# Kernel optimization log

Measured on AMD Instinct MI355X. Metric: run time of the kernel, lower is better.

The kernel has to match this reference:

```python
import jax, jax.numpy as jnp
import numpy as np

F = 26          # field_size
D = 16          # embed_dim
B = 16384       # batch
VOCABS = [1000] * F
OFFSETS = np.concatenate([[0], np.cumsum(VOCABS)[:-1]]).astype(np.int32)
IU, JU = np.triu_indices(F, k=1)   # 325 pairs (i<j)
P = IU.shape[0]
BN_EPS = 1e-3   # Keras BatchNormalization default epsilon


def setup_inputs() -> dict:
    key = jax.random.key(0)
    ks = jax.random.split(key, 8)
    s = 0.05  # keras 'random_normal' initializer stddev
    return {
        "x": jax.random.randint(ks[0], (B, F), 0, 1000, dtype=jnp.int32),
        "emb_table": jax.random.normal(ks[1], (sum(VOCABS) + 1, D), jnp.float32) * s,
        "se_w1": jax.random.normal(ks[2], (F, F // 2), jnp.float32) * s,
        "se_w2": jax.random.normal(ks[3], (F // 2, F), jnp.float32) * s,
        "bl_w": jax.random.normal(ks[4], (P, D, D), jnp.float32) * s,
        "w1": jax.random.normal(ks[5], (F * (F - 1) * D, 64), jnp.float32) * s,
        "b1": jnp.zeros((64,), jnp.float32),
        "g1": jnp.ones((64,), jnp.float32),
        "be1": jnp.zeros((64,), jnp.float32),
        "m1": jnp.zeros((64,), jnp.float32),
        "v1": jnp.ones((64,), jnp.float32),
        "w2": jax.random.normal(ks[6], (64, 32), jnp.float32) * s,
        "b2": jnp.zeros((32,), jnp.float32),
        "g2": jnp.ones((32,), jnp.float32),
        "be2": jnp.zeros((32,), jnp.float32),
        "m2": jnp.zeros((32,), jnp.float32),
        "v2": jnp.ones((32,), jnp.float32),
        "w3": jax.random.normal(ks[7], (32, 1), jnp.float32) * s,
        "b3": jnp.zeros((1,), jnp.float32),
    }


def _bilinear(v, bl_w):
    # v: [B, F, D]; shared W stack over the 325 ordered pairs (i<j)
    # tmp[p] = (v_i @ W_p) * v_j  -> [B, P, D]
    return jnp.einsum('bpd,pde->bpe', v[:, IU], bl_w) * v[:, JU]


def _bn(h, g, b, m, v):
    return g * (h - m) * jax.lax.rsqrt(v + BN_EPS) + b


def reference(x, emb_table, se_w1, se_w2, bl_w,
              w1, b1, g1, be1, m1, v1,
              w2, b2, g2, be2, m2, v2,
              w3, b3):
    ids = x + jnp.asarray(OFFSETS)
    e = emb_table[ids]                         # [B, F, D]
    # SE layer: mean-pool over embed dim, two ReLU dense layers, rescale
    z = e.mean(axis=-1)                        # [B, F]
    A = jax.nn.relu(jax.nn.relu(z @ se_w1) @ se_w2)
    se = e * A[..., None]                      # [B, F, D]
    # Bilinear interaction (same weights for both calls)
    p = _bilinear(e, bl_w).reshape(e.shape[0], -1)     # [B, P*D]
    se_p = _bilinear(se, bl_w).reshape(e.shape[0], -1)
    h = jnp.concatenate([p, se_p], axis=-1)    # [B, F*(F-1)*D]
    # MLP with inference-mode BatchNorm; dropout=0 is a no-op
    h = jax.nn.relu(_bn(h @ w1 + b1, g1, be1, m1, v1))
    h = jax.nn.relu(_bn(h @ w2 + b2, g2, be2, m2, v2))
    return jax.nn.sigmoid(h @ w3 + b3)         # [B, 1]
```

## Files before the change

kernel.cpp:

```cpp
#include <hip/hip_runtime.h>
#include <cstdint>
#include <cstddef>


#define F_FIELDS 26
#define P_PAIRS 325
#define PAD_PAIRS 336
#define BATCH 16384
#define BN_EPS 1e-3f
#define ROWS 64

typedef short bf16x8 __attribute__((ext_vector_type(8)));
typedef float f32x4 __attribute__((ext_vector_type(4)));
typedef int   i32x4 __attribute__((ext_vector_type(4)));

struct PairTab { unsigned char iu[PAD_PAIRS]; unsigned char ju[PAD_PAIRS]; };
static constexpr PairTab make_pairs() {
    PairTab t{};
    int p = 0;
    for (int a = 0; a < F_FIELDS; ++a)
        for (int b = a + 1; b < F_FIELDS; ++b) { t.iu[p] = (unsigned char)a; t.ju[p] = (unsigned char)b; ++p; }
    for (; p < PAD_PAIRS; ++p) { t.iu[p] = 0; t.ju[p] = 0; }
    return t;
}
__constant__ PairTab PT = make_pairs();

__device__ __forceinline__ unsigned short bf16u(float v) {
    unsigned u = __float_as_uint(v);
    unsigned r = (u + 0x7fffu + ((u >> 16) & 1u)) >> 16;
    return (unsigned short)r;
}
__device__ __forceinline__ unsigned pk_bf16(float lo, float hi) {
    return (unsigned)bf16u(lo) | ((unsigned)bf16u(hi) << 16);
}
__device__ __forceinline__ float bflo(unsigned d) { return __uint_as_float(d << 16); }
__device__ __forceinline__ float bfhi(unsigned d) { return __uint_as_float(d & 0xffff0000u); }
__device__ __forceinline__ unsigned pk_trunc(float u, float cu) {
    return __builtin_amdgcn_perm(__float_as_uint(cu), __float_as_uint(u), 0x07060302u);
}

__global__ __launch_bounds__(256) void k_wprep(const float* __restrict__ w1,
        const float* __restrict__ blw, unsigned short* __restrict__ w1catL,
        unsigned short* __restrict__ wcatL) {
    const int p = blockIdx.x;
    const int tid = threadIdx.x;
    if (p >= P_PAIRS) {
        int4 z = make_int4(0, 0, 0, 0);
        *(int4*)(w1catL + (size_t)p * 2048 + tid * 8) = z;
        if (tid < 64) *(int4*)(wcatL + (size_t)p * 512 + tid * 8) = z;
        return;
    }
    __shared__ float wu[1024], wv[1024], wb[256];
    ((float4*)wu)[tid] = ((const float4*)(w1 + (size_t)p * 1024))[tid];
    ((float4*)wv)[tid] = ((const float4*)(w1 + 332800 + (size_t)p * 1024))[tid];
    if (tid < 64) ((float4*)wb)[tid] = ((const float4*)(blw + (size_t)p * 256))[tid];
    __syncthreads();
    {
        int nt = tid >> 6, lane = tid & 63, ln = lane & 15, q = lane >> 4;
        int o = nt * 16 + ln;
        unsigned short outv[8];
        #pragma unroll
        for (int j = 0; j < 8; ++j) {
            int k = q * 8 + j, d = k >> 1, su = k & 1;
            outv[j] = bf16u(su ? wv[d * 64 + o] : wu[d * 64 + o]);
        }
        *(int4*)(w1catL + (size_t)p * 2048 + tid * 8) = *(const int4*)outv;
    }
    if (tid < 64) {
        int ln = tid & 15, q = tid >> 4;
        unsigned short outv[8];
        #pragma unroll
        for (int j = 0; j < 8; ++j) {
            int din = q * 8 + j;
            outv[j] = (din < 16) ? bf16u(wb[din * 16 + ln]) : (unsigned short)0;
        }
        *(int4*)(wcatL + (size_t)p * 512 + tid * 8) = *(const int4*)outv;
    }
}

union __align__(16) SMem {
    struct {
        unsigned short eS[ROWS * 424];
        float aS[F_FIELDS * ROWS];
    } a;
    struct {
        unsigned ysh[8 * 8 * 64 * 4];
        float h1s[ROWS * 65];
        float h2s[ROWS * 36];
    } b;
};

#define ISSUE_W(pp, waS, wbS0, wbS1, wbS2, wbS3) do {                                   \
    const unsigned short* ba_ = wcatL + (size_t)(pp) * 512 + lane * 8;                  \
    const unsigned short* bb_ = w1catL + (size_t)(pp) * 2048 + lane * 8;                \
    asm volatile("global_load_dwordx4 %0, %1, off"             : "=v"(waS)  : "v"(ba_)); \
    asm volatile("global_load_dwordx4 %0, %1, off"             : "=v"(wbS0) : "v"(bb_)); \
    asm volatile("global_load_dwordx4 %0, %1, off offset:1024" : "=v"(wbS1) : "v"(bb_)); \
    asm volatile("global_load_dwordx4 %0, %1, off offset:2048" : "=v"(wbS2) : "v"(bb_)); \
    asm volatile("global_load_dwordx4 %0, %1, off offset:3072" : "=v"(wbS3) : "v"(bb_)); \
} while (0)

#define PAIR_BODY(p_, waS, wbS0, wbS1, wbS2, wbS3, waT, wbT0, wbT1, wbT2, wbT3) do {    \
    const int pn_ = ((p_) + 1 < p1) ? (p_) + 1 : (p1 - 1);                              \
    const int pf_ = ((p_) + 2 < p1) ? (p_) + 2 : (p1 - 1);                              \
    const int ju_ = PT.ju[p_];                                                          \
    uint2 ejv_[4]; float cv_[4];                                                        \
    _Pragma("unroll") for (int mt = 0; mt < 4; ++mt) {                                  \
        ejv_[mt] = *(const uint2*)(eS + (mt * 16 + ln) * 424 + ju_ * 16 + q * 4);       \
        cv_[mt]  = ai[mt] * aS[ju_ * ROWS + mt * 16 + ln];                              \
    }                                                                                   \
    const int iun_ = PT.iu[pn_];                                                        \
    if (iun_ != iu_c) {                                                                 \
        iu_c = iun_;                                                                    \
        _Pragma("unroll") for (int mt = 0; mt < 4; ++mt) {                              \
            eiB[mt] = __builtin_bit_cast(bf16x8,                                        \
                *(const int4*)(eS + (mt * 16 + ln) * 424 + iu_c * 16 + (q & 1) * 8));   \
            ai[mt] = aS[iu_c * ROWS + mt * 16 + ln];                                    \
        }                                                                               \
    }                                                                                   \
    bf16x8 wbv_[4] = { __builtin_bit_cast(bf16x8, wbS0), __builtin_bit_cast(bf16x8, wbS1), \
                       __builtin_bit_cast(bf16x8, wbS2), __builtin_bit_cast(bf16x8, wbS3) }; \
    _Pragma("unroll") for (int mt = 0; mt < 4; ++mt) {                                  \
        f32x4 t = tc[mt];                                                               \
        float e0 = bflo(ejv_[mt].x), e1 = bfhi(ejv_[mt].x);                             \
        float e2 = bflo(ejv_[mt].y), e3 = bfhi(ejv_[mt].y);                             \
        float c  = cv_[mt];                                                             \
        float u0 = t[0] * e0, u1 = t[1] * e1, u2 = t[2] * e2, u3 = t[3] * e3;           \
        int4 af;                                                                        \
        af.x = (int)pk_trunc(u0, c * u0);                                               \
        af.y = (int)pk_trunc(u1, c * u1);                                               \
        af.z = (int)pk_trunc(u2, c * u2);                                               \
        af.w = (int)pk_trunc(u3, c * u3);                                               \
        bf16x8 A_ = __builtin_bit_cast(bf16x8, af);                                     \
        _Pragma("unroll") for (int nt = 0; nt < 4; ++nt)                                \
            acc[mt][nt] = __builtin_amdgcn_mfma_f32_16x16x32_bf16(A_, wbv_[nt], acc[mt][nt], 0, 0, 0); \
    }                                                                                   \
    ISSUE_W(pf_, waS, wbS0, wbS1, wbS2, wbS3);                                          \
    asm volatile("s_waitcnt vmcnt(5)" ::: "memory");                                    \
    __builtin_amdgcn_sched_barrier(0);                                                  \
    {                                                                                   \
        bf16x8 waT_ = __builtin_bit_cast(bf16x8, waT);                                  \
        _Pragma("unroll") for (int mt = 0; mt < 4; ++mt)                                \
            tc[mt] = __builtin_amdgcn_mfma_f32_16x16x32_bf16(waT_, eiB[mt], zero4, 0, 0, 0); \
    }                                                                                   \
} while (0)

__global__ __launch_bounds__(512, 2) void k_main(const int* __restrict__ x,
        const float* __restrict__ emb, const float* __restrict__ sw1,
        const float* __restrict__ sw2, const unsigned short* __restrict__ w1catL,
        const unsigned short* __restrict__ wcatL,
        const float* __restrict__ b1, const float* __restrict__ g1,
        const float* __restrict__ be1, const float* __restrict__ m1,
        const float* __restrict__ v1,
        const float* __restrict__ w2, const float* __restrict__ b2,
        const float* __restrict__ g2, const float* __restrict__ be2,
        const float* __restrict__ m2, const float* __restrict__ v2,
        const float* __restrict__ w3, const float* __restrict__ b3,
        float* __restrict__ out) {
    __shared__ SMem sm;
    __shared__ float z_s[ROWS][F_FIELDS];
    __shared__ float sw1_s[F_FIELDS * 13];
    __shared__ float sw2_s[13 * F_FIELDS];
    const int tid = threadIdx.x;
    const int b0 = blockIdx.x * ROWS;
    unsigned short* eS = sm.a.eS;
    float* aS = sm.a.aS;

    for (int i = tid; i < F_FIELDS * 13; i += 512) { sw1_s[i] = sw1[i]; sw2_s[i] = sw2[i]; }
    for (int idx = tid; idx < ROWS * F_FIELDS; idx += 512) {
        int r = idx / F_FIELDS, f = idx - r * F_FIELDS;
        int id = x[(b0 + r) * F_FIELDS + f] + f * 1000;
        const float4* src = (const float4*)(emb + (size_t)id * 16);
        float4 v0 = src[0], v1l = src[1], v2l = src[2], v3l = src[3];
        int4 o0, o1;
        o0.x = (int)pk_bf16(v0.x, v0.y);  o0.y = (int)pk_bf16(v0.z, v0.w);
        o0.z = (int)pk_bf16(v1l.x, v1l.y); o0.w = (int)pk_bf16(v1l.z, v1l.w);
        o1.x = (int)pk_bf16(v2l.x, v2l.y); o1.y = (int)pk_bf16(v2l.z, v2l.w);
        o1.z = (int)pk_bf16(v3l.x, v3l.y); o1.w = (int)pk_bf16(v3l.z, v3l.w);
        *(int4*)(eS + r * 424 + f * 16) = o0;
        *(int4*)(eS + r * 424 + f * 16 + 8) = o1;
        float s = v0.x + v0.y + v0.z + v0.w + v1l.x + v1l.y + v1l.z + v1l.w
                + v2l.x + v2l.y + v2l.z + v2l.w + v3l.x + v3l.y + v3l.z + v3l.w;
        z_s[r][f] = s * (1.0f / 16.0f);
    }
    __syncthreads();
    if (tid < ROWS) {
        float s1[13];
        #pragma unroll
        for (int o = 0; o < 13; ++o) {
            float acc0 = 0.f;
            #pragma unroll
            for (int f = 0; f < F_FIELDS; ++f) acc0 = fmaf(z_s[tid][f], sw1_s[f * 13 + o], acc0);
            s1[o] = fmaxf(acc0, 0.0f);
        }
        #pragma unroll
        for (int f = 0; f < F_FIELDS; ++f) {
            float acc0 = 0.f;
            #pragma unroll
            for (int o = 0; o < 13; ++o) acc0 = fmaf(s1[o], sw2_s[o * F_FIELDS + f], acc0);
            aS[f * ROWS + tid] = fmaxf(acc0, 0.0f);
        }
    }
    __syncthreads();

    const int w    = tid >> 6;
    const int lane = tid & 63;
    const int ln   = lane & 15;
    const int q    = lane >> 4;
    const int p0 = w * 42, p1 = p0 + 42;

    f32x4 acc[4][4];
    #pragma unroll
    for (int a = 0; a < 4; ++a)
        #pragma unroll
        for (int b = 0; b < 4; ++b) acc[a][b] = (f32x4){0.f, 0.f, 0.f, 0.f};
    const f32x4 zero4 = {0.f, 0.f, 0.f, 0.f};

    int iu_c = PT.iu[p0];
    bf16x8 eiB[4];
    float ai[4];
    #pragma unroll
    for (int mt = 0; mt < 4; ++mt) {
        eiB[mt] = __builtin_bit_cast(bf16x8,
            *(const int4*)(eS + (mt * 16 + ln) * 424 + iu_c * 16 + (q & 1) * 8));
        ai[mt] = aS[iu_c * ROWS + mt * 16 + ln];
    }

    i32x4 waA, wbA0, wbA1, wbA2, wbA3;
    i32x4 waB, wbB0, wbB1, wbB2, wbB3;
    ISSUE_W(p0,     waA, wbA0, wbA1, wbA2, wbA3);
    ISSUE_W(p0 + 1, waB, wbB0, wbB1, wbB2, wbB3);
    asm volatile("s_waitcnt vmcnt(5)" ::: "memory");
    __builtin_amdgcn_sched_barrier(0);

    f32x4 tc[4];
    {
        bf16x8 waA_ = __builtin_bit_cast(bf16x8, waA);
        #pragma unroll
        for (int mt = 0; mt < 4; ++mt)
            tc[mt] = __builtin_amdgcn_mfma_f32_16x16x32_bf16(waA_, eiB[mt], zero4, 0, 0, 0);
    }

    for (int p = p0; p < p1; p += 2) {
        PAIR_BODY(p,     waA, wbA0, wbA1, wbA2, wbA3, waB, wbB0, wbB1, wbB2, wbB3);
        PAIR_BODY(p + 1, waB, wbB0, wbB1, wbB2, wbB3, waA, wbA0, wbA1, wbA2, wbA3);
    }
    asm volatile("s_waitcnt vmcnt(0)" ::: "memory");
    __builtin_amdgcn_sched_barrier(0);

    __syncthreads();
    unsigned* ysh = sm.b.ysh;
    float* h1s = sm.b.h1s;
    float* h2s = sm.b.h2s;
    #pragma unroll
    for (int mt = 0; mt < 4; ++mt)
        #pragma unroll
        for (int nh = 0; nh < 2; ++nh) {
            int nt0 = nh * 2, nt1 = nh * 2 + 1;
            int4 v;
            v.x = (int)pk_bf16(acc[mt][nt0][0], acc[mt][nt0][1]);
            v.y = (int)pk_bf16(acc[mt][nt0][2], acc[mt][nt0][3]);
            v.z = (int)pk_bf16(acc[mt][nt1][0], acc[mt][nt1][1]);
            v.w = (int)pk_bf16(acc[mt][nt1][2], acc[mt][nt1][3]);
            *(int4*)(ysh + ((w * 8 + mt * 2 + nh) * 64 + lane) * 4) = v;
        }
    __syncthreads();

    {
        const int s = tid >> 6, lane2 = tid & 63, ln2 = lane2 & 15, q2 = lane2 >> 4;
        const int mt = s >> 1, nh = s & 1;
        const int c0 = nh * 32 + ln2, c1 = c0 + 16;
        const float sc0 = g1[c0] * rsqrtf(v1[c0] + BN_EPS);
        const float of0 = be1[c0] + sc0 * (b1[c0] - m1[c0]);
        const float sc1 = g1[c1] * rsqrtf(v1[c1] + BN_EPS);
        const float of1 = be1[c1] + sc1 * (b1[c1] - m1[c1]);
        float s8[8];
        #pragma unroll
        for (int i = 0; i < 8; ++i) s8[i] = 0.f;
        #pragma unroll
        for (int wv = 0; wv < 8; ++wv) {
            int4 v = *(const int4*)(ysh + ((wv * 8 + s) * 64 + lane2) * 4);
            s8[0] += bflo((unsigned)v.x); s8[1] += bfhi((unsigned)v.x);
            s8[2] += bflo((unsigned)v.y); s8[3] += bfhi((unsigned)v.y);
            s8[4] += bflo((unsigned)v.z); s8[5] += bfhi((unsigned)v.z);
            s8[6] += bflo((unsigned)v.w); s8[7] += bfhi((unsigned)v.w);
        }
        const int row0 = mt * 16 + q2 * 4;
        #pragma unroll
        for (int r = 0; r < 4; ++r) {
            h1s[(row0 + r) * 65 + c0] = fmaxf(s8[r] * sc0 + of0, 0.f);
            h1s[(row0 + r) * 65 + c1] = fmaxf(s8[4 + r] * sc1 + of1, 0.f);
        }
    }
    __syncthreads();

    {
        const int row = tid >> 3, gg = tid & 7;
        const int o0 = gg * 4;
        float a0 = 0.f, a1 = 0.f, a2 = 0.f, a3 = 0.f;
        #pragma unroll 8
        for (int k = 0; k < 64; ++k) {
            float hk = h1s[row * 65 + k];
            float4 wv = *(const float4*)(w2 + k * 32 + o0);
            a0 = fmaf(hk, wv.x, a0);
            a1 = fmaf(hk, wv.y, a1);
            a2 = fmaf(hk, wv.z, a2);
            a3 = fmaf(hk, wv.w, a3);
        }
        const float4 g2v  = *(const float4*)(g2 + o0);
        const float4 b2v  = *(const float4*)(b2 + o0);
        const float4 m2v  = *(const float4*)(m2 + o0);
        const float4 v2v  = *(const float4*)(v2 + o0);
        const float4 be2v = *(const float4*)(be2 + o0);
        float4 hv;
        hv.x = fmaxf(g2v.x * (a0 + b2v.x - m2v.x) * rsqrtf(v2v.x + BN_EPS) + be2v.x, 0.f);
        hv.y = fmaxf(g2v.y * (a1 + b2v.y - m2v.y) * rsqrtf(v2v.y + BN_EPS) + be2v.y, 0.f);
        hv.z = fmaxf(g2v.z * (a2 + b2v.z - m2v.z) * rsqrtf(v2v.z + BN_EPS) + be2v.z, 0.f);
        hv.w = fmaxf(g2v.w * (a3 + b2v.w - m2v.w) * rsqrtf(v2v.w + BN_EPS) + be2v.w, 0.f);
        *(float4*)(h2s + row * 36 + o0) = hv;
    }
    __syncthreads();
    if (tid < ROWS) {
        float sacc = b3[0];
        #pragma unroll
        for (int k = 0; k < 32; ++k) sacc = fmaf(h2s[tid * 36 + k], w3[k], sacc);
        out[b0 + tid] = 1.0f / (1.0f + expf(-sacc));
    }
}

extern "C" void kernel_launch(void* const* d_in, const int* in_sizes, int n_in,
                              void* d_out, int out_size, void* d_ws, size_t ws_size,
                              hipStream_t stream) {
    const int*   x   = (const int*)d_in[0];
    const float* emb = (const float*)d_in[1];
    const float* sw1 = (const float*)d_in[2];
    const float* sw2 = (const float*)d_in[3];
    const float* blw = (const float*)d_in[4];
    const float* w1  = (const float*)d_in[5];
    const float* b1  = (const float*)d_in[6];
    const float* g1  = (const float*)d_in[7];
    const float* be1 = (const float*)d_in[8];
    const float* m1  = (const float*)d_in[9];
    const float* v1  = (const float*)d_in[10];
    const float* w2  = (const float*)d_in[11];
    const float* b2  = (const float*)d_in[12];
    const float* g2  = (const float*)d_in[13];
    const float* be2 = (const float*)d_in[14];
    const float* m2  = (const float*)d_in[15];
    const float* v2  = (const float*)d_in[16];
    const float* w3  = (const float*)d_in[17];
    const float* b3  = (const float*)d_in[18];
    float* out = (float*)d_out;

    char* ws = (char*)d_ws;
    unsigned short* w1catL = (unsigned short*)ws;
    unsigned short* wcatL  = (unsigned short*)(ws + 1376256);

    hipLaunchKernelGGL(k_wprep, dim3(PAD_PAIRS), dim3(256), 0, stream, w1, blw, w1catL, wcatL);
    hipLaunchKernelGGL(k_main,  dim3(BATCH / ROWS), dim3(512), 0, stream,
                       x, emb, sw1, sw2, w1catL, wcatL,
                       b1, g1, be1, m1, v1, w2, b2, g2, be2, m2, v2, w3, b3, out);
}
```

Baseline: 137.2 us.

## Split each wave's pair loop into two interleaved independent streams

Each wave's 42 pairs are split into two halves of 21, processed as two interleaved streams (A and B) with separate first-stage results, embeddings and weight registers. This is meant to give the scheduler independent MFMA chains to overlap with latency. Pair indices are now advanced incrementally instead of read from the constant table, and hand-written asm loads with explicit waitcnt are replaced by plain loads that prefetch one step ahead. s_setprio is raised around the MFMA block. The cost is higher register pressure from duplicated state, plus dependence on the compiler to schedule loads well.

```diff
diff --git a/kernel.cpp b/kernel.cpp
--- a/kernel.cpp
+++ b/kernel.cpp
@@ -9,10 +9,10 @@
 #define BATCH 16384
 #define BN_EPS 1e-3f
 #define ROWS 64
+#define PPH 21
 
 typedef short bf16x8 __attribute__((ext_vector_type(8)));
 typedef float f32x4 __attribute__((ext_vector_type(4)));
-typedef int   i32x4 __attribute__((ext_vector_type(4)));
 
 struct PairTab { unsigned char iu[PAD_PAIRS]; unsigned char ju[PAD_PAIRS]; };
 static constexpr PairTab make_pairs() {
@@ -90,41 +90,38 @@
     } b;
 };
 
-#define ISSUE_W(pp, waS, wbS0, wbS1, wbS2, wbS3) do {                                   \
-    const unsigned short* ba_ = wcatL + (size_t)(pp) * 512 + lane * 8;                  \
-    const unsigned short* bb_ = w1catL + (size_t)(pp) * 2048 + lane * 8;                \
-    asm volatile("global_load_dwordx4 %0, %1, off"             : "=v"(waS)  : "v"(ba_)); \
-    asm volatile("global_load_dwordx4 %0, %1, off"             : "=v"(wbS0) : "v"(bb_)); \
-    asm volatile("global_load_dwordx4 %0, %1, off offset:1024" : "=v"(wbS1) : "v"(bb_)); \
-    asm volatile("global_load_dwordx4 %0, %1, off offset:2048" : "=v"(wbS2) : "v"(bb_)); \
-    asm volatile("global_load_dwordx4 %0, %1, off offset:3072" : "=v"(wbS3) : "v"(bb_)); \
-} while (0)
-
-#define PAIR_BODY(p_, waS, wbS0, wbS1, wbS2, wbS3, waT, wbT0, wbT1, wbT2, wbT3) do {    \
-    const int pn_ = ((p_) + 1 < p1) ? (p_) + 1 : (p1 - 1);                              \
-    const int pf_ = ((p_) + 2 < p1) ? (p_) + 2 : (p1 - 1);                              \
-    const int ju_ = PT.ju[p_];                                                          \
-    uint2 ejv_[4]; float cv_[4];                                                        \
+#define STREAM_STEP(iu_, ju_, ei_, ai_, wa_, wb_, tc_, pn_) do {                        \
+    bf16x8 wa_n = __builtin_bit_cast(bf16x8, *(const int4*)(wcatL + (size_t)(pn_) * 512 + lane * 8)); \
+    bf16x8 wb_n0 = __builtin_bit_cast(bf16x8, *(const int4*)(w1catL + (size_t)(pn_) * 2048 + 0 * 512 + lane * 8)); \
+    bf16x8 wb_n1 = __builtin_bit_cast(bf16x8, *(const int4*)(w1catL + (size_t)(pn_) * 2048 + 1 * 512 + lane * 8)); \
+    bf16x8 wb_n2 = __builtin_bit_cast(bf16x8, *(const int4*)(w1catL + (size_t)(pn_) * 2048 + 2 * 512 + lane * 8)); \
+    bf16x8 wb_n3 = __builtin_bit_cast(bf16x8, *(const int4*)(w1catL + (size_t)(pn_) * 2048 + 3 * 512 + lane * 8)); \
+    const int ju = ju_;                                                                 \
+    uint2 ejv[4]; float cv[4];                                                          \
     _Pragma("unroll") for (int mt = 0; mt < 4; ++mt) {                                  \
-        ejv_[mt] = *(const uint2*)(eS + (mt * 16 + ln) * 424 + ju_ * 16 + q * 4);       \
-        cv_[mt]  = ai[mt] * aS[ju_ * ROWS + mt * 16 + ln];                              \
+        ejv[mt] = *(const uint2*)(eS + (mt * 16 + ln) * 424 + ju * 16 + q * 4);         \
+        cv[mt]  = ai_[mt] * aS[ju * ROWS + mt * 16 + ln];                               \
     }                                                                                   \
-    const int iun_ = PT.iu[pn_];                                                        \
-    if (iun_ != iu_c) {                                                                 \
-        iu_c = iun_;                                                                    \
+    const int iu_prev = iu_;                                                            \
+    ++ju_;                                                                              \
+    if (ju_ == F_FIELDS) {                                                              \
+        ++iu_;                                                                          \
+        if (iu_ >= F_FIELDS - 1) iu_ = 0;                                               \
+        ju_ = iu_ + 1;                                                                  \
+    }                                                                                   \
+    if (iu_ != iu_prev) {                                                               \
         _Pragma("unroll") for (int mt = 0; mt < 4; ++mt) {                              \
-            eiB[mt] = __builtin_bit_cast(bf16x8,                                        \
-                *(const int4*)(eS + (mt * 16 + ln) * 424 + iu_c * 16 + (q & 1) * 8));   \
-            ai[mt] = aS[iu_c * ROWS + mt * 16 + ln];                                    \
+            ei_[mt] = __builtin_bit_cast(bf16x8,                                        \
+                *(const int4*)(eS + (mt * 16 + ln) * 424 + iu_ * 16 + (q & 1) * 8));    \
+            ai_[mt] = aS[iu_ * ROWS + mt * 16 + ln];                                    \
         }                                                                               \
     }                                                                                   \
-    bf16x8 wbv_[4] = { __builtin_bit_cast(bf16x8, wbS0), __builtin_bit_cast(bf16x8, wbS1), \
-                       __builtin_bit_cast(bf16x8, wbS2), __builtin_bit_cast(bf16x8, wbS3) }; \
+    __builtin_amdgcn_s_setprio(1);                                                      \
     _Pragma("unroll") for (int mt = 0; mt < 4; ++mt) {                                  \
-        f32x4 t = tc[mt];                                                               \
-        float e0 = bflo(ejv_[mt].x), e1 = bfhi(ejv_[mt].x);                             \
-        float e2 = bflo(ejv_[mt].y), e3 = bfhi(ejv_[mt].y);                             \
-        float c  = cv_[mt];                                                             \
+        f32x4 t = tc_[mt];                                                              \
+        float e0 = bflo(ejv[mt].x), e1 = bfhi(ejv[mt].x);                               \
+        float e2 = bflo(ejv[mt].y), e3 = bfhi(ejv[mt].y);                               \
+        float c  = cv[mt];                                                              \
         float u0 = t[0] * e0, u1 = t[1] * e1, u2 = t[2] * e2, u3 = t[3] * e3;           \
         int4 af;                                                                        \
         af.x = (int)pk_trunc(u0, c * u0);                                               \
@@ -132,17 +129,16 @@
         af.z = (int)pk_trunc(u2, c * u2);                                               \
         af.w = (int)pk_trunc(u3, c * u3);                                               \
         bf16x8 A_ = __builtin_bit_cast(bf16x8, af);                                     \
-        _Pragma("unroll") for (int nt = 0; nt < 4; ++nt)                                \
-            acc[mt][nt] = __builtin_amdgcn_mfma_f32_16x16x32_bf16(A_, wbv_[nt], acc[mt][nt], 0, 0, 0); \
+        acc[mt][0] = __builtin_amdgcn_mfma_f32_16x16x32_bf16(A_, wb_[0], acc[mt][0], 0, 0, 0); \
+        acc[mt][1] = __builtin_amdgcn_mfma_f32_16x16x32_bf16(A_, wb_[1], acc[mt][1], 0, 0, 0); \
+        acc[mt][2] = __builtin_amdgcn_mfma_f32_16x16x32_bf16(A_, wb_[2], acc[mt][2], 0, 0, 0); \
+        acc[mt][3] = __builtin_amdgcn_mfma_f32_16x16x32_bf16(A_, wb_[3], acc[mt][3], 0, 0, 0); \
     }                                                                                   \
-    ISSUE_W(pf_, waS, wbS0, wbS1, wbS2, wbS3);                                          \
-    asm volatile("s_waitcnt vmcnt(5)" ::: "memory");                                    \
-    __builtin_amdgcn_sched_barrier(0);                                                  \
-    {                                                                                   \
-        bf16x8 waT_ = __builtin_bit_cast(bf16x8, waT);                                  \
-        _Pragma("unroll") for (int mt = 0; mt < 4; ++mt)                                \
-            tc[mt] = __builtin_amdgcn_mfma_f32_16x16x32_bf16(waT_, eiB[mt], zero4, 0, 0, 0); \
-    }                                                                                   \
+    _Pragma("unroll") for (int mt = 0; mt < 4; ++mt)                                    \
+        tc_[mt] = __builtin_amdgcn_mfma_f32_16x16x32_bf16(wa_n, ei_[mt], zero4, 0, 0, 0); \
+    __builtin_amdgcn_s_setprio(0);                                                      \
+    wa_ = wa_n;                                                                         \
+    wb_[0] = wb_n0; wb_[1] = wb_n1; wb_[2] = wb_n2; wb_[3] = wb_n3;                     \
 } while (0)
 
 __global__ __launch_bounds__(512, 2) void k_main(const int* __restrict__ x,
@@ -203,11 +199,12 @@
     }
     __syncthreads();
 
-    const int w    = tid >> 6;
+    const int w    = __builtin_amdgcn_readfirstlane(tid >> 6);
     const int lane = tid & 63;
     const int ln   = lane & 15;
     const int q    = lane >> 4;
-    const int p0 = w * 42, p1 = p0 + 42;
+    const int p0A = w * 42;
+    const int p0B = w * 42 + PPH;
 
     f32x4 acc[4][4];
     #pragma unroll
@@ -216,37 +213,49 @@
         for (int b = 0; b < 4; ++b) acc[a][b] = (f32x4){0.f, 0.f, 0.f, 0.f};
     const f32x4 zero4 = {0.f, 0.f, 0.f, 0.f};
 
-    int iu_c = PT.iu[p0];
-    bf16x8 eiB[4];
-    float ai[4];
+    int iuA = PT.iu[p0A], juA = PT.ju[p0A];
+    bf16x8 eA[4]; float aiA[4];
     #pragma unroll
     for (int mt = 0; mt < 4; ++mt) {
-        eiB[mt] = __builtin_bit_cast(bf16x8,
-            *(const int4*)(eS + (mt * 16 + ln) * 424 + iu_c * 16 + (q & 1) * 8));
-        ai[mt] = aS[iu_c * ROWS + mt * 16 + ln];
-    }
-
-    i32x4 waA, wbA0, wbA1, wbA2, wbA3;
-    i32x4 waB, wbB0, wbB1, wbB2, wbB3;
-    ISSUE_W(p0,     waA, wbA0, wbA1, wbA2, wbA3);
-    ISSUE_W(p0 + 1, waB, wbB0, wbB1, wbB2, wbB3);
-    asm volatile("s_waitcnt vmcnt(5)" ::: "memory");
-    __builtin_amdgcn_sched_barrier(0);
-
-    f32x4 tc[4];
-    {
-        bf16x8 waA_ = __builtin_bit_cast(bf16x8, waA);
-        #pragma unroll
-        for (int mt = 0; mt < 4; ++mt)
-            tc[mt] = __builtin_amdgcn_mfma_f32_16x16x32_bf16(waA_, eiB[mt], zero4, 0, 0, 0);
-    }
-
-    for (int p = p0; p < p1; p += 2) {
-        PAIR_BODY(p,     waA, wbA0, wbA1, wbA2, wbA3, waB, wbB0, wbB1, wbB2, wbB3);
-        PAIR_BODY(p + 1, waB, wbB0, wbB1, wbB2, wbB3, waA, wbA0, wbA1, wbA2, wbA3);
-    }
-    asm volatile("s_waitcnt vmcnt(0)" ::: "memory");
-    __builtin_amdgcn_sched_barrier(0);
+        eA[mt] = __builtin_bit_cast(bf16x8,
+            *(const int4*)(eS + (mt * 16 + ln) * 424 + iuA * 16 + (q & 1) * 8));
+        aiA[mt] = aS[iuA * ROWS + mt * 16 + ln];
+    }
+    bf16x8 waA = __builtin_bit_cast(bf16x8, *(const int4*)(wcatL + (size_t)p0A * 512 + lane * 8));
+    bf16x8 wbA[4];
+    #pragma unroll
+    for (int nt = 0; nt < 4; ++nt)
+        wbA[nt] = __builtin_bit_cast(bf16x8, *(const int4*)(w1catL + (size_t)p0A * 2048 + nt * 512 + lane * 8));
+    f32x4 tcA[4];
+    #pragma unroll
+    for (int mt = 0; mt < 4; ++mt)
+        tcA[mt] = __builtin_amdgcn_mfma_f32_16x16x32_bf16(waA, eA[mt], zero4, 0, 0, 0);
+
+    int iuB = PT.iu[p0B], juB = PT.ju[p0B];
+    bf16x8 eB[4]; float aiB[4];
+    #pragma unroll
+    for (int mt = 0; mt < 4; ++mt) {
+        eB[mt] = __builtin_bit_cast(bf16x8,
+            *(const int4*)(eS + (mt * 16 + ln) * 424 + iuB * 16 + (q & 1) * 8));
+        aiB[mt] = aS[iuB * ROWS + mt * 16 + ln];
+    }
+    bf16x8 waB = __builtin_bit_cast(bf16x8, *(const int4*)(wcatL + (size_t)p0B * 512 + lane * 8));
+    bf16x8 wbB[4];
+    #pragma unroll
+    for (int nt = 0; nt < 4; ++nt)
+        wbB[nt] = __builtin_bit_cast(bf16x8, *(const int4*)(w1catL + (size_t)p0B * 2048 + nt * 512 + lane * 8));
+    f32x4 tcB[4];
+    #pragma unroll
+    for (int mt = 0; mt < 4; ++mt)
+        tcB[mt] = __builtin_amdgcn_mfma_f32_16x16x32_bf16(waB, eB[mt], zero4, 0, 0, 0);
+
+    #pragma unroll 1
+    for (int i = 0; i < PPH; ++i) {
+        const int pnA = (i + 1 < PPH) ? (p0A + i + 1) : (p0A + PPH - 1);
+        const int pnB = (i + 1 < PPH) ? (p0B + i + 1) : (p0B + PPH - 1);
+        STREAM_STEP(iuA, juA, eA, aiA, waA, wbA, tcA, pnA);
+        STREAM_STEP(iuB, juB, eB, aiB, waB, wbB, tcB, pnB);
+    }
 
     __syncthreads();
     unsigned* ysh = sm.b.ysh;
```

New measurement: 132.6 us. -3.4%, faster.
